# Optimization experiments

Hardware: AMD Instinct MI355X
Metric: run time of the kernel (lower is better)

Reference implementation:

```python
import jax, jax.numpy as jnp
import numpy as np

RANGES = (1, 2, 4, 10, 25)
B, L, D, V = 64, 1000, 300, 50000  # L divisible by every r in RANGES -> no remainder group


def setup_inputs() -> dict:
    key = jax.random.key(0)
    ks = jax.random.split(key, 12)
    u = lambda k, s: jax.random.uniform(k, s, dtype=jnp.float32) / 6  # matches torch.rand(...)/6
    return {
        "article_in": jax.random.randint(ks[0], (B, L), 0, V),
        "emb": jax.random.normal(ks[1], (V, D), dtype=jnp.float32) * 0.02,
        "w_ce": u(ks[2], (len(RANGES), D, D)),   # per-range W in contract-expand
        "b_ce": u(ks[3], (len(RANGES), 1, D)),   # per-range b (shape (1,D) in source)
        "w1": u(ks[4], (3, len(RANGES))),
        "b1": u(ks[5], (3, D)),
        "w2": u(ks[6], (1, 3)),
        "b2": u(ks[7], (1, D)),
        "wz": u(ks[8], (D, D)),
        "bz": u(ks[9], (1, D)),
        "wo": u(ks[10], (D, D)),
        "bo": u(ks[11], (1, D)),
    }


def _mru(x, w_ce, b_ce, w1, b1, w2, b2, wz, bz, wo, bo):
    b, l, d = x.shape
    # --- contract-expand: segment-sum windows of size r, tiny matmul, broadcast back /r ---
    ce = []
    for i, r in enumerate(RANGES):
        seg = x.reshape(b, l // r, r, d).sum(axis=2)                 # [B, L/r, D] segment sums
        t = jax.nn.relu(seg @ w_ce[i]) + b_ce[i]                     # relu(sum @ W) + b
        ce.append(jnp.repeat(t, r, axis=1) / r)                      # expand each group back, divided by r
    pre = jnp.stack(ce, axis=2)                                      # [B, L, 5, D]
    # --- multi-ranged reasoning MLP across the 5 ranges ---
    h1 = jax.nn.relu(jnp.einsum('ts,blsd->bltd', w1, pre) + b1)      # [B, L, 3, D]
    gate = jax.nn.relu(jnp.einsum('ot,bltd->blod', w2, h1) + b2)[:, :, 0, :]  # [B, L, D]
    # --- gated recurrent encoding (note: bias added OUTSIDE tanh, per source) ---
    z = jnp.tanh(x @ wz) + bz                                        # [B, L, D]
    o = jnp.tanh(x @ wo) + bo                                        # [B, L, D]

    def step(c, inp):
        g, zt, ot = inp
        c = g * c + (1.0 - g) * zt
        return c, ot * c

    seq = (gate.transpose(1, 0, 2), z.transpose(1, 0, 2), o.transpose(1, 0, 2))  # [L, B, D]
    _, h = jax.lax.scan(step, jnp.zeros((b, d), x.dtype), seq)
    return h.transpose(1, 0, 2)                                      # [B, L, D]


def reference(article_in, emb, w_ce, b_ce, w1, b1, w2, b2, wz, bz, wo, bo):
    x = emb[article_in]                                              # embedding lookup [B, L, D]
    return _mru(x, w_ce, b_ce, w1, b1, w2, b2, wz, bz, wo, bo)
```

## Files before the change

### kernel.cpp

```cpp
#include <hip/hip_runtime.h>
#include <hip/hip_bf16.h>

typedef unsigned short u16;
typedef unsigned int   u32;
typedef __attribute__((ext_vector_type(8))) short short8;
typedef __attribute__((ext_vector_type(4))) float floatx4;
typedef __attribute__((ext_vector_type(4))) unsigned short u16x4;

__device__ __forceinline__ u16 f2bf(float f){
  u32 x = __float_as_uint(f);
  u32 r = (x + 0x7fffu + ((x >> 16) & 1u)) >> 16;
  return (u16)r;
}
__device__ __forceinline__ float bf2f(u16 u){
  return __uint_as_float(((u32)u) << 16);
}
__device__ __forceinline__ float tanh_fast(float x){
  float xs = fminf(fmaxf(x, -16.f), 16.f);
  float e  = __builtin_amdgcn_exp2f(xs * 2.8853900817779268f);
  return (e - 1.f) * __builtin_amdgcn_rcpf(e + 1.f);
}
__device__ __forceinline__ void gload16(const void* g, void* l){
  __builtin_amdgcn_global_load_lds(
      (const __attribute__((address_space(1))) unsigned int*)g,
      (__attribute__((address_space(3))) unsigned int*)l, 16, 0, 0);
}

__global__ void k_gather_seg(const int* __restrict__ idx, const float* __restrict__ emb,
                             u16* __restrict__ x, u16* __restrict__ s2,
                             u16* __restrict__ s4, u16* __restrict__ s10, int total){
  int i = blockIdx.x * blockDim.x + threadIdx.x;
  if (i >= total) return;
  int d4 = i % 80; int rest = i / 80; int w = rest % 50; int b = rest / 50;
  const int dcol = d4 * 4;
  const int r0 = b * 1000 + w * 20;
  float a2[4] = {0,0,0,0}, a4[4] = {0,0,0,0}, a10[4] = {0,0,0,0};
  #pragma unroll
  for (int j = 0; j < 20; j++){
    const int r = r0 + j;
    u16x4 o; o[0] = 0; o[1] = 0; o[2] = 0; o[3] = 0;
    if (d4 < 75){
      const float4 v = *(const float4*)(emb + (size_t)idx[r] * 300 + dcol);
      o[0] = f2bf(v.x); o[1] = f2bf(v.y); o[2] = f2bf(v.z); o[3] = f2bf(v.w);
      a2[0] += v.x; a2[1] += v.y; a2[2] += v.z; a2[3] += v.w;
      a4[0] += v.x; a4[1] += v.y; a4[2] += v.z; a4[3] += v.w;
      a10[0] += v.x; a10[1] += v.y; a10[2] += v.z; a10[3] += v.w;
    }
    *(u16x4*)(x + (size_t)r * 320 + dcol) = o;
    if (j & 1){
      u16x4 s;
      #pragma unroll
      for (int q = 0; q < 4; q++){ s[q] = f2bf(a2[q]); a2[q] = 0.f; }
      *(u16x4*)(s2 + ((size_t)(b * 500 + w * 10 + (j >> 1)) * 320 + dcol)) = s;
    }
    if ((j & 3) == 3){
      u16x4 s;
      #pragma unroll
      for (int q = 0; q < 4; q++){ s[q] = f2bf(a4[q]); a4[q] = 0.f; }
      *(u16x4*)(s4 + ((size_t)(b * 250 + w * 5 + (j >> 2)) * 320 + dcol)) = s;
    }
    if (j == 9 || j == 19){
      u16x4 s;
      #pragma unroll
      for (int q = 0; q < 4; q++){ s[q] = f2bf(a10[q]); a10[q] = 0.f; }
      *(u16x4*)(s10 + ((size_t)(b * 100 + w * 2 + j / 10) * 320 + dcol)) = s;
    }
  }
}

__global__ void k_s25(const u16* __restrict__ x, u16* __restrict__ s25, int total){
  int i = blockIdx.x * blockDim.x + threadIdx.x;
  if (i >= total) return;
  int d4 = i % 80; int rest = i / 80; int g = rest % 40; int b = rest / 40;
  const int dcol = d4 * 4;
  const u16* src = x + ((size_t)(b * 1000 + g * 25) * 320 + dcol);
  float a[4] = {0,0,0,0};
  #pragma unroll
  for (int j = 0; j < 25; j++){
    u16x4 v = *(const u16x4*)(src + (size_t)j * 320);
    #pragma unroll
    for (int q = 0; q < 4; q++) a[q] += bf2f(v[q]);
  }
  u16x4 o;
  #pragma unroll
  for (int q = 0; q < 4; q++) o[q] = f2bf(a[q]);
  *(u16x4*)(s25 + ((size_t)(b * 40 + g) * 320 + dcol)) = o;
}

__global__ void k_wprep(const float* __restrict__ wce, const float* __restrict__ wz,
                        const float* __restrict__ wo, u16* __restrict__ wT, int total){
  int i = blockIdx.x * blockDim.x + threadIdx.x;
  if (i >= total) return;
  int mat = i / 102400; int rem = i - mat * 102400;
  int n = rem / 320;    int k = rem - n * 320;
  float v = 0.f;
  if (n < 300 && k < 300){
    const float* src = (mat < 5) ? (wce + mat * 90000) : (mat == 5 ? wz : wo);
    v = src[k * 300 + n];
  }
  wT[i] = f2bf(v);
}

__global__ __launch_bounds__(512, 2) void k_gemm_all(
    const u16* __restrict__ x,  const u16* __restrict__ s2,
    const u16* __restrict__ s4, const u16* __restrict__ s10,
    const u16* __restrict__ s25,const u16* __restrict__ wT,
    u16* __restrict__ t0, u16* __restrict__ t1, u16* __restrict__ t2,
    u16* __restrict__ t3, u16* __restrict__ t4,
    u16* __restrict__ zb, u16* __restrict__ ob,
    const float* __restrict__ b_ce, const float* __restrict__ bz,
    const float* __restrict__ bo)
{
  __shared__ __align__(16) char lds[57344];

  const int bid = blockIdx.x;
  const u16 *A, *BT; u16* C; const float* bias;
  int mode; float scale; long tileRow;
  if (bid < 1512){
    const int xcd = bid & 7, j = bid >> 3;
    const int T = (j / 3) * 8 + xcd, m = j % 3;
    if (T >= 500) return;
    tileRow = (long)T * 128; A = x;
    if (m == 0)      { BT = wT;              C = t0; bias = b_ce; mode = 0; scale = 1.f; }
    else if (m == 1) { BT = wT + 5 * 102400; C = zb; bias = bz;   mode = 1; scale = 1.f; }
    else             { BT = wT + 6 * 102400; C = ob; bias = bo;   mode = 1; scale = 1.f; }
  } else {
    const int g = bid - 1512;
    if (g < 250)      { A=s2;  BT=wT+1*102400; C=t1; bias=b_ce+300;  mode=0; scale=0.5f;  tileRow=(long)g*128; }
    else if (g < 375) { A=s4;  BT=wT+2*102400; C=t2; bias=b_ce+600;  mode=0; scale=0.25f; tileRow=(long)(g-250)*128; }
    else if (g < 425) { A=s10; BT=wT+3*102400; C=t3; bias=b_ce+900;  mode=0; scale=0.1f;  tileRow=(long)(g-375)*128; }
    else              { A=s25; BT=wT+4*102400; C=t4; bias=b_ce+1200; mode=0; scale=0.04f; tileRow=(long)(g-425)*128; }
  }

  const int tid  = threadIdx.x;
  const int lane = tid & 63;
  const int wid  = tid >> 6;
  const int wr   = wid >> 2;
  const int wc   = wid & 3;
  const int L    = lane & 15;
  const int kc   = lane >> 4;

  const int arow = tid >> 2, ac = tid & 3;
  const u16* aSrc = A + (tileRow + arow) * 320 + ((ac ^ ((arow >> 1) & 3)) << 3);
  const u16* bSrc[3];
  #pragma unroll
  for (int l = 0; l < 3; l++){
    const int idx2 = l * 512 + tid, col = idx2 >> 2, cc = idx2 & 3;
    bSrc[l] = BT + col * 320 + ((cc ^ ((col >> 1) & 3)) << 3);
  }
  const int wbase = wid * 1024;

  const int rA   = wr * 64 + L;
  const int cB   = wc * 80 + L;
  const int kchA = (kc ^ ((rA >> 1) & 3)) << 4;
  const int kchB = (kc ^ ((cB >> 1) & 3)) << 4;

  floatx4 acc[4][5];
  #pragma unroll
  for (int m = 0; m < 4; m++)
    #pragma unroll
    for (int n = 0; n < 5; n++)
      #pragma unroll
      for (int q = 0; q < 4; q++) acc[m][n][q] = 0.f;

  #define STAGE(t, nb) do {                                                    \
    gload16(aSrc + (t) * 32, lds + (nb) * 8192 + wbase);                       \
    gload16(bSrc[0] + (t) * 32, lds + 16384 + (nb) * 20480 + wbase);           \
    gload16(bSrc[1] + (t) * 32, lds + 16384 + (nb) * 20480 + 8192 + wbase);    \
    if (tid < 256)                                                             \
      gload16(bSrc[2] + (t) * 32, lds + 16384 + (nb) * 20480 + 16384 + wbase); \
  } while (0)

  STAGE(0, 0);
  __syncthreads();

  #pragma unroll
  for (int t = 0; t < 10; t++){
    const int cur = t & 1;
    if (t < 9) STAGE(t + 1, cur ^ 1);
    const char* Ab = lds + cur * 8192;
    const char* Bb = lds + 16384 + cur * 20480;
    short8 af[4], bf[5];
    #pragma unroll
    for (int m = 0; m < 4; m++)
      af[m] = *(const short8*)(Ab + (rA + m * 16) * 64 + kchA);
    #pragma unroll
    for (int n = 0; n < 5; n++)
      bf[n] = *(const short8*)(Bb + (cB + n * 16) * 64 + kchB);
    #pragma unroll
    for (int m = 0; m < 4; m++)
      #pragma unroll
      for (int n = 0; n < 5; n++)
        acc[m][n] = __builtin_amdgcn_mfma_f32_16x16x32_bf16(af[m], bf[n], acc[m][n], 0, 0, 0);
    __syncthreads();
  }
  #undef STAGE

  const int colbase = wc * 80 + L;
  const long rowb   = tileRow + wr * 64 + (kc << 2);
  #pragma unroll
  for (int m = 0; m < 4; m++){
    #pragma unroll
    for (int n = 0; n < 5; n++){
      const int gcol = colbase + n * 16;
      if (gcol < 300){
        const float bv = bias[gcol];
        #pragma unroll
        for (int r = 0; r < 4; r++){
          const long grow = rowb + m * 16 + r;
          float v = acc[m][n][r];
          v = (mode == 0) ? (fmaxf(v, 0.f) + bv) * scale : tanh_fast(v) + bv;
          C[grow * 300 + gcol] = f2bf(v);
        }
      }
    }
  }
}

__device__ __forceinline__ float gate_eval(
    float p0, float p1, float p2, float p3, float p4,
    const float W1[3][5], const float W2[3], const float B1[3], float B2)
{
  float acc2 = B2;
  #pragma unroll
  for (int t = 0; t < 3; t++){
    float u = W1[t][0]*p0 + W1[t][1]*p1 + W1[t][2]*p2 + W1[t][3]*p3 + W1[t][4]*p4 + B1[t];
    acc2 += W2[t] * fmaxf(u, 0.f);
  }
  return fmaxf(acc2, 0.f);
}

__global__ void k_scan1(const u16* __restrict__ t0, const u16* __restrict__ t1,
    const u16* __restrict__ t2, const u16* __restrict__ t3, const u16* __restrict__ t4,
    const u16* __restrict__ z,
    const float* __restrict__ w1, const float* __restrict__ b1,
    const float* __restrict__ w2, const float* __restrict__ b2,
    float* __restrict__ cA, float* __restrict__ cB, int total)
{
  int i = blockIdx.x * blockDim.x + threadIdx.x;
  if (i >= total) return;
  int d4 = i % 75; int rest = i / 75; int ch = rest % 40; int b = rest / 40;
  const int d = d4 * 4;
  float W1[3][5], W2[3], B1[3][4], B2[4];
  #pragma unroll
  for (int t = 0; t < 3; t++){
    #pragma unroll
    for (int s = 0; s < 5; s++) W1[t][s] = w1[t * 5 + s];
    W2[t] = w2[t];
    #pragma unroll
    for (int q = 0; q < 4; q++) B1[t][q] = b1[t * 300 + d + q];
  }
  #pragma unroll
  for (int q = 0; q < 4; q++) B2[q] = b2[d + q];
  float Ac[4] = {1.f,1.f,1.f,1.f}, Bc[4] = {0.f,0.f,0.f,0.f};
  const int l0 = ch * 25;
  const u16x4 v4 = *(const u16x4*)(t4 + (size_t)(b * 40 + ch) * 300 + d);
  for (int l = l0; l < l0 + 25; l++){
    u16x4 v0 = *(const u16x4*)(t0 + (size_t)(b * 1000 + l)        * 300 + d);
    u16x4 v1 = *(const u16x4*)(t1 + (size_t)(b * 500  + (l >> 1)) * 300 + d);
    u16x4 v2 = *(const u16x4*)(t2 + (size_t)(b * 250  + (l >> 2)) * 300 + d);
    u16x4 v3 = *(const u16x4*)(t3 + (size_t)(b * 100  + l / 10)   * 300 + d);
    u16x4 vz = *(const u16x4*)(z  + (size_t)(b * 1000 + l)        * 300 + d);
    #pragma unroll
    for (int q = 0; q < 4; q++){
      float B1q[3] = {B1[0][q], B1[1][q], B1[2][q]};
      float g  = gate_eval(bf2f(v0[q]), bf2f(v1[q]), bf2f(v2[q]), bf2f(v3[q]), bf2f(v4[q]),
                           W1, W2, B1q, B2[q]);
      Ac[q] = g * Ac[q];
      Bc[q] = g * Bc[q] + (1.f - g) * bf2f(vz[q]);
    }
  }
  *(float4*)(cA + (size_t)ch * 19200 + b * 300 + d) = make_float4(Ac[0], Ac[1], Ac[2], Ac[3]);
  *(float4*)(cB + (size_t)ch * 19200 + b * 300 + d) = make_float4(Bc[0], Bc[1], Bc[2], Bc[3]);
}

__global__ void k_scan2(const float* __restrict__ cA, const float* __restrict__ cB,
                        float* __restrict__ cinit, int total){
  int i = blockIdx.x * blockDim.x + threadIdx.x;
  if (i >= total) return;
  float c = 0.f;
  for (int ch = 0; ch < 40; ch++){
    cinit[ch * 19200 + i] = c;
    c = cA[ch * 19200 + i] * c + cB[ch * 19200 + i];
  }
}

__global__ void k_scan3(const u16* __restrict__ t0, const u16* __restrict__ t1,
    const u16* __restrict__ t2, const u16* __restrict__ t3, const u16* __restrict__ t4,
    const u16* __restrict__ z, const u16* __restrict__ o,
    const float* __restrict__ cinit,
    const float* __restrict__ w1, const float* __restrict__ b1,
    const float* __restrict__ w2, const float* __restrict__ b2,
    float* __restrict__ out, int total)
{
  int i = blockIdx.x * blockDim.x + threadIdx.x;
  if (i >= total) return;
  int d4 = i % 75; int rest = i / 75; int ch = rest % 40; int b = rest / 40;
  const int d = d4 * 4;
  float W1[3][5], W2[3], B1[3][4], B2[4];
  #pragma unroll
  for (int t = 0; t < 3; t++){
    #pragma unroll
    for (int s = 0; s < 5; s++) W1[t][s] = w1[t * 5 + s];
    W2[t] = w2[t];
    #pragma unroll
    for (int q = 0; q < 4; q++) B1[t][q] = b1[t * 300 + d + q];
  }
  #pragma unroll
  for (int q = 0; q < 4; q++) B2[q] = b2[d + q];
  float c[4];
  {
    float4 ci = *(const float4*)(cinit + (size_t)ch * 19200 + b * 300 + d);
    c[0] = ci.x; c[1] = ci.y; c[2] = ci.z; c[3] = ci.w;
  }
  const int l0 = ch * 25;
  const u16x4 v4 = *(const u16x4*)(t4 + (size_t)(b * 40 + ch) * 300 + d);
  for (int l = l0; l < l0 + 25; l++){
    u16x4 v0 = *(const u16x4*)(t0 + (size_t)(b * 1000 + l)        * 300 + d);
    u16x4 v1 = *(const u16x4*)(t1 + (size_t)(b * 500  + (l >> 1)) * 300 + d);
    u16x4 v2 = *(const u16x4*)(t2 + (size_t)(b * 250  + (l >> 2)) * 300 + d);
    u16x4 v3 = *(const u16x4*)(t3 + (size_t)(b * 100  + l / 10)   * 300 + d);
    u16x4 vz = *(const u16x4*)(z  + (size_t)(b * 1000 + l)        * 300 + d);
    u16x4 vo = *(const u16x4*)(o  + (size_t)(b * 1000 + l)        * 300 + d);
    float4 res;
    #pragma unroll
    for (int q = 0; q < 4; q++){
      float B1q[3] = {B1[0][q], B1[1][q], B1[2][q]};
      float g  = gate_eval(bf2f(v0[q]), bf2f(v1[q]), bf2f(v2[q]), bf2f(v3[q]), bf2f(v4[q]),
                           W1, W2, B1q, B2[q]);
      c[q] = g * c[q] + (1.f - g) * bf2f(vz[q]);
      ((float*)&res)[q] = bf2f(vo[q]) * c[q];
    }
    *(float4*)(out + (size_t)(b * 1000 + l) * 300 + d) = res;
  }
}

extern "C" void kernel_launch(void* const* d_in, const int* in_sizes, int n_in,
                              void* d_out, int out_size, void* d_ws, size_t ws_size,
                              hipStream_t stream){
  const int*   article = (const int*)  d_in[0];
  const float* emb     = (const float*)d_in[1];
  const float* w_ce    = (const float*)d_in[2];
  const float* b_ce    = (const float*)d_in[3];
  const float* w1      = (const float*)d_in[4];
  const float* b1      = (const float*)d_in[5];
  const float* w2      = (const float*)d_in[6];
  const float* b2      = (const float*)d_in[7];
  const float* wz      = (const float*)d_in[8];
  const float* bz      = (const float*)d_in[9];
  const float* wo      = (const float*)d_in[10];
  const float* bo      = (const float*)d_in[11];
  float* out = (float*)d_out;
  char*  ws  = (char*)d_ws;

  u16* x    = (u16*)(ws + 0UL);
  u16* s2   = (u16*)(ws + 40960000UL);
  u16* s4   = (u16*)(ws + 61440000UL);
  u16* s10  = (u16*)(ws + 71680000UL);
  u16* s25  = (u16*)(ws + 75776000UL);
  u16* wT   = (u16*)(ws + 77414400UL);
  u16* t0   = (u16*)(ws + 78848000UL);
  u16* t1   = (u16*)(ws + 117248000UL);
  u16* t2   = (u16*)(ws + 136448000UL);
  u16* t3   = (u16*)(ws + 146048000UL);
  u16* t4   = (u16*)(ws + 149888000UL);
  u16* zb   = (u16*)(ws + 151424000UL);
  u16* ob   = (u16*)(ws + 189824000UL);
  float* cA = (float*)(ws + 40960000UL);
  float* cB = (float*)(ws + 44032000UL);
  float* ci = (float*)(ws + 47104000UL);
  (void)ws_size; (void)in_sizes; (void)n_in; (void)out_size;

  k_wprep     <<<2800, 256, 0, stream>>>(w_ce, wz, wo, wT, 716800);
  k_gather_seg<<<1000, 256, 0, stream>>>(article, emb, x, s2, s4, s10, 256000);
  k_s25       <<< 800, 256, 0, stream>>>(x, s25, 204800);

  k_gemm_all<<<1957, 512, 0, stream>>>(x, s2, s4, s10, s25, wT,
                                       t0, t1, t2, t3, t4, zb, ob,
                                       b_ce, bz, bo);

  k_scan1<<<750, 256, 0, stream>>>(t0, t1, t2, t3, t4, zb, w1, b1, w2, b2, cA, cB, 192000);
  k_scan2<<< 75, 256, 0, stream>>>(cA, cB, ci, 19200);
  k_scan3<<<750, 256, 0, stream>>>(t0, t1, t2, t3, t4, zb, ob, ci, w1, b1, w2, b2, out, 192000);
}
```

Before: 238.9 us.

## Use 64-wide K stages, XOR swizzle, and transposed MFMA for vectorized stores

Doubles the K-slice per pipeline stage from 32 to 64, so the GEMM runs 5 iterations with half as many barriers. This doubles LDS to 112 KB and uses an 8-way XOR swizzle on the 128-byte rows. The MFMA operands are swapped so each lane holds 4 consecutive output columns, which turns the epilogue into 8-byte bf16 vector stores with float4 bias loads. The larger LDS footprint may cut occupancy below the 2 blocks per CU that the launch bounds request.

```diff
diff --git a/kernel.cpp b/kernel.cpp
--- a/kernel.cpp
+++ b/kernel.cpp
@@ -111,7 +111,7 @@
     const float* __restrict__ b_ce, const float* __restrict__ bz,
     const float* __restrict__ bo)
 {
-  __shared__ __align__(16) char lds[57344];
+  __shared__ __align__(16) char lds[114688];
 
   const int bid = blockIdx.x;
   const u16 *A, *BT; u16* C; const float* bias;
@@ -137,23 +137,28 @@
   const int wid  = tid >> 6;
   const int wr   = wid >> 2;
   const int wc   = wid & 3;
-  const int L    = lane & 15;
-  const int kc   = lane >> 4;
-
-  const int arow = tid >> 2, ac = tid & 3;
-  const u16* aSrc = A + (tileRow + arow) * 320 + ((ac ^ ((arow >> 1) & 3)) << 3);
-  const u16* bSrc[3];
-  #pragma unroll
-  for (int l = 0; l < 3; l++){
-    const int idx2 = l * 512 + tid, col = idx2 >> 2, cc = idx2 & 3;
-    bSrc[l] = BT + col * 320 + ((cc ^ ((col >> 1) & 3)) << 3);
-  }
-  const int wbase = wid * 1024;
-
-  const int rA   = wr * 64 + L;
-  const int cB   = wc * 80 + L;
-  const int kchA = (kc ^ ((rA >> 1) & 3)) << 4;
-  const int kchB = (kc ^ ((cB >> 1) & 3)) << 4;
+
+  const u16* aSrc[2]; int aDst[2];
+  #pragma unroll
+  for (int l = 0; l < 2; l++){
+    const int idx = l * 512 + tid, row = idx >> 3, c = idx & 7;
+    aSrc[l] = A + (tileRow + row) * 320 + ((c ^ (row & 7)) << 3);
+    aDst[l] = (l * 512 + wid * 64) * 16;
+  }
+  const u16* bSrc[5]; int bDst[5];
+  #pragma unroll
+  for (int l = 0; l < 5; l++){
+    const int idx = l * 512 + tid, col = idx >> 3, c = idx & 7;
+    bSrc[l] = BT + col * 320 + ((c ^ (col & 7)) << 3);
+    bDst[l] = (l * 512 + wid * 64) * 16;
+  }
+
+  const int rA  = wr * 64 + (lane & 15);
+  const int cBt = wc * 80 + (lane & 15);
+  int ksw[2];
+  #pragma unroll
+  for (int s = 0; s < 2; s++)
+    ksw[s] = ((s * 4 + (lane >> 4)) ^ (lane & 7)) << 4;
 
   floatx4 acc[4][5];
   #pragma unroll
@@ -163,55 +168,62 @@
       #pragma unroll
       for (int q = 0; q < 4; q++) acc[m][n][q] = 0.f;
 
-  #define STAGE(t, nb) do {                                                    \
-    gload16(aSrc + (t) * 32, lds + (nb) * 8192 + wbase);                       \
-    gload16(bSrc[0] + (t) * 32, lds + 16384 + (nb) * 20480 + wbase);           \
-    gload16(bSrc[1] + (t) * 32, lds + 16384 + (nb) * 20480 + 8192 + wbase);    \
-    if (tid < 256)                                                             \
-      gload16(bSrc[2] + (t) * 32, lds + 16384 + (nb) * 20480 + 16384 + wbase); \
-  } while (0)
-
-  STAGE(0, 0);
+  #pragma unroll
+  for (int l = 0; l < 2; l++) gload16(aSrc[l], lds + aDst[l]);
+  #pragma unroll
+  for (int l = 0; l < 5; l++) gload16(bSrc[l], lds + 32768 + bDst[l]);
   __syncthreads();
 
   #pragma unroll
-  for (int t = 0; t < 10; t++){
+  for (int t = 0; t < 5; t++){
     const int cur = t & 1;
-    if (t < 9) STAGE(t + 1, cur ^ 1);
-    const char* Ab = lds + cur * 8192;
-    const char* Bb = lds + 16384 + cur * 20480;
-    short8 af[4], bf[5];
-    #pragma unroll
-    for (int m = 0; m < 4; m++)
-      af[m] = *(const short8*)(Ab + (rA + m * 16) * 64 + kchA);
-    #pragma unroll
-    for (int n = 0; n < 5; n++)
-      bf[n] = *(const short8*)(Bb + (cB + n * 16) * 64 + kchB);
-    #pragma unroll
-    for (int m = 0; m < 4; m++)
+    if (t < 4){
+      const int nb = cur ^ 1;
+      #pragma unroll
+      for (int l = 0; l < 2; l++) gload16(aSrc[l] + (t + 1) * 64, lds + nb * 16384 + aDst[l]);
+      #pragma unroll
+      for (int l = 0; l < 5; l++) gload16(bSrc[l] + (t + 1) * 64, lds + 32768 + nb * 40960 + bDst[l]);
+    }
+    const char* bA = lds + cur * 16384;
+    const char* bB = lds + 32768 + cur * 40960;
+    #pragma unroll
+    for (int s = 0; s < 2; s++){
+      short8 af[4], bf[5];
+      #pragma unroll
+      for (int m = 0; m < 4; m++)
+        af[m] = *(const short8*)(bA + (rA + m * 16) * 128 + ksw[s]);
       #pragma unroll
       for (int n = 0; n < 5; n++)
-        acc[m][n] = __builtin_amdgcn_mfma_f32_16x16x32_bf16(af[m], bf[n], acc[m][n], 0, 0, 0);
+        bf[n] = *(const short8*)(bB + (cBt + n * 16) * 128 + ksw[s]);
+      #pragma unroll
+      for (int m = 0; m < 4; m++)
+        #pragma unroll
+        for (int n = 0; n < 5; n++)
+          acc[m][n] = __builtin_amdgcn_mfma_f32_16x16x32_bf16(bf[n], af[m], acc[m][n], 0, 0, 0);
+    }
     __syncthreads();
   }
-  #undef STAGE
-
-  const int colbase = wc * 80 + L;
-  const long rowb   = tileRow + wr * 64 + (kc << 2);
-  #pragma unroll
-  for (int m = 0; m < 4; m++){
-    #pragma unroll
-    for (int n = 0; n < 5; n++){
-      const int gcol = colbase + n * 16;
-      if (gcol < 300){
-        const float bv = bias[gcol];
+
+  const int L  = lane & 15;
+  const int kc = lane >> 4;
+  const long rowb = tileRow + wr * 64 + L;
+  #pragma unroll
+  for (int n = 0; n < 5; n++){
+    const int gcol = wc * 80 + n * 16 + kc * 4;
+    if (gcol < 300){
+      const float4 bv4 = *(const float4*)(bias + gcol);
+      #pragma unroll
+      for (int m = 0; m < 4; m++){
+        const long grow = rowb + m * 16;
+        u16x4 st;
         #pragma unroll
         for (int r = 0; r < 4; r++){
-          const long grow = rowb + m * 16 + r;
           float v = acc[m][n][r];
+          const float bv = ((const float*)&bv4)[r];
           v = (mode == 0) ? (fmaxf(v, 0.f) + bv) * scale : tanh_fast(v) + bv;
-          C[grow * 300 + gcol] = f2bf(v);
+          st[r] = f2bf(v);
         }
+        *(u16x4*)(C + (size_t)grow * 300 + gcol) = st;
       }
     }
   }
```

Measured after the change: 229.1 us. 1.04x faster.
